# Performance work log

Hardware: AMD Instinct MI355X
Metric: run time of the kernel (lower is better)

Reference implementation:

```python
import jax, jax.numpy as jnp
import numpy as np

N_BITS = 8
QMAX = 2 ** (N_BITS - 1) - 1  # 127 for int8 symmetric


def fake_quant(x):
    """Per-token (last-dim) dynamic symmetric fake quantization (quant->dequant)."""
    scale = jnp.max(jnp.abs(x), axis=-1, keepdims=True) / QMAX
    scale = jnp.maximum(scale, 1e-8)
    q = jnp.clip(jnp.round(x / scale), -QMAX - 1, QMAX)
    return q * scale


def setup_inputs() -> dict:
    key = jax.random.key(0)
    k1, k2, k3, k4, k5 = jax.random.split(key, 5)
    B, T, D, H = 32, 1024, 1152, 4608
    x = jax.random.normal(k1, (B, T, D), dtype=jnp.float32)
    reorder_index = jnp.arange(D, dtype=jnp.int32)  # channel reorder permutation
    W1 = jax.random.normal(k2, (H, D), dtype=jnp.float32) * (1.0 / np.sqrt(D))
    b1 = jax.random.normal(k3, (H,), dtype=jnp.float32) * 0.02
    W2 = jax.random.normal(k4, (D, H), dtype=jnp.float32) * (1.0 / np.sqrt(H))
    b2 = jax.random.normal(k5, (D,), dtype=jnp.float32) * 0.02
    return {"x": x, "reorder_index": reorder_index, "W1": W1, "b1": b1, "W2": W2, "b2": b2}


def reference(x, reorder_index, W1, b1, W2, b2):
    # channel reorder (index_select on dim 2)
    x = jnp.take(x, reorder_index, axis=2)
    # input fake-quant
    x = fake_quant(x)
    # fc1 (torch Linear: x @ W.T + b)
    h = jnp.einsum("btd,hd->bth", x, W1) + b1
    # GELU activation (timm Mlp default); drop1/norm are Identity in eval
    h = jax.nn.gelu(h, approximate=False)
    # activation fake-quant
    h = fake_quant(h)
    # fc2
    out = jnp.einsum("bth,dh->btd", h, W2) + b2
    return out
```

## Files before the change

kernel.cpp:

```cpp
#include <hip/hip_runtime.h>
#include <cstdint>
#include <cstddef>


typedef __attribute__((ext_vector_type(8))) short short8;
typedef __attribute__((ext_vector_type(4))) float f32x4;

__device__ __forceinline__ float bf2f(unsigned short u) {
    return __uint_as_float(((unsigned)u) << 16);
}
__device__ __forceinline__ unsigned short f2bf(float f) {
    unsigned u = __float_as_uint(f);
    u += 0x7fff + ((u >> 16) & 1);
    return (unsigned short)(u >> 16);
}

__device__ __forceinline__ void gload_lds16(const void* gptr, void* ldsptr) {
    typedef __attribute__((address_space(1))) const unsigned int gu32;
    typedef __attribute__((address_space(3))) unsigned int lu32;
    __builtin_amdgcn_global_load_lds((gu32*)gptr, (lu32*)ldsptr, 16, 0, 0);
}

template <bool GELU>
__global__ __launch_bounds__(256) void gemm_bt(
    const unsigned short* __restrict__ A, const unsigned short* __restrict__ B,
    const float* __restrict__ bias, const float* __restrict__ rowScale,
    void* __restrict__ C, int M, int N, int K)
{
    __shared__ unsigned short lA[128 * 64];
    __shared__ unsigned short lB[128 * 64];

    const int tid  = threadIdx.x;
    const int lane = tid & 63;
    const int wave = tid >> 6;
    const int wm = wave >> 1;
    const int wn = wave & 1;
    const int bn = blockIdx.x;
    const int bm = blockIdx.y;

    const unsigned short* Ab = A + (size_t)bm * 128 * K;
    const unsigned short* Bb = B + (size_t)bn * 128 * K;

    f32x4 acc[4][4];
    const f32x4 zero = {0.f, 0.f, 0.f, 0.f};
#pragma unroll
    for (int i = 0; i < 4; ++i)
#pragma unroll
        for (int j = 0; j < 4; ++j) acc[i][j] = zero;

    const int q  = lane >> 4;
    const int lr = lane & 15;
    const int wbase = tid & 0xFFC0;

    const int nk = K >> 6;
    for (int kb = 0; kb < nk; ++kb) {
        const unsigned short* Ak = Ab + kb * 64;
        const unsigned short* Bk = Bb + kb * 64;
#pragma unroll
        for (int i = 0; i < 4; ++i) {
            int idx = i * 256 + tid;
            int r = idx >> 3, sc = idx & 7;
            int c = (sc ^ (r & 7)) << 3;
            gload_lds16(Ak + (size_t)r * K + c, &lA[(i * 256 + wbase) * 8]);
        }
#pragma unroll
        for (int i = 0; i < 4; ++i) {
            int idx = i * 256 + tid;
            int r = idx >> 3, sc = idx & 7;
            int c = (sc ^ (r & 7)) << 3;
            gload_lds16(Bk + (size_t)r * K + c, &lB[(i * 256 + wbase) * 8]);
        }
        __syncthreads();

#pragma unroll
        for (int ks = 0; ks < 2; ++ks) {
            short8 af[4], bfr[4];
            const int c8 = ks * 4 + q;
#pragma unroll
            for (int i = 0; i < 4; ++i) {
                int R = wm * 64 + i * 16 + lr;
                af[i] = *(const short8*)&lA[R * 64 + ((c8 ^ (R & 7)) << 3)];
            }
#pragma unroll
            for (int j = 0; j < 4; ++j) {
                int R = wn * 64 + j * 16 + lr;
                bfr[j] = *(const short8*)&lB[R * 64 + ((c8 ^ (R & 7)) << 3)];
            }
#pragma unroll
            for (int i = 0; i < 4; ++i)
#pragma unroll
                for (int j = 0; j < 4; ++j)
                    acc[i][j] = __builtin_amdgcn_mfma_f32_16x16x32_bf16(
                        af[i], bfr[j], acc[i][j], 0, 0, 0);
        }
        __syncthreads();
    }

#pragma unroll
    for (int i = 0; i < 4; ++i) {
#pragma unroll
        for (int r = 0; r < 4; ++r) {
            int m = bm * 128 + wm * 64 + i * 16 + q * 4 + r;
            float sc = rowScale[m];
#pragma unroll
            for (int j = 0; j < 4; ++j) {
                int n = bn * 128 + wn * 64 + j * 16 + lr;
                float v = acc[i][j][r] * sc + bias[n];
                size_t off = (size_t)m * N + n;
                if (GELU) {
                    v = 0.5f * v * (1.f + erff(v * 0.70710678118654752f));
                    ((unsigned short*)C)[off] = f2bf(v);
                } else {
                    ((float*)C)[off] = v;
                }
            }
        }
    }
}

__device__ __forceinline__ float waveMax(float m) {
#pragma unroll
    for (int off = 32; off; off >>= 1) m = fmaxf(m, __shfl_xor(m, off));
    return m;
}

__global__ __launch_bounds__(256) void quant_x_kernel(
    const float* __restrict__ x, const int* __restrict__ ridx,
    unsigned short* __restrict__ xq, float* __restrict__ sx, int D)
{
    __shared__ float buf[1152];
    __shared__ float wmax[4];
    const float* xr = x + (size_t)blockIdx.x * D;
    const int tid = threadIdx.x;
    float m = 0.f;
    for (int c = tid; c < D; c += 256) {
        float v = xr[ridx[c]];
        buf[c] = v;
        m = fmaxf(m, fabsf(v));
    }
    m = waveMax(m);
    if ((tid & 63) == 0) wmax[tid >> 6] = m;
    __syncthreads();
    m = fmaxf(fmaxf(wmax[0], wmax[1]), fmaxf(wmax[2], wmax[3]));
    float scale = fmaxf(m * (1.f / 127.f), 1e-8f);
    float inv = 1.f / scale;
    unsigned short* xo = xq + (size_t)blockIdx.x * D;
    for (int c = tid; c < D; c += 256) {
        float qv = fminf(fmaxf(rintf(buf[c] * inv), -128.f), 127.f);
        xo[c] = f2bf(qv);
    }
    if (tid == 0) sx[blockIdx.x] = scale;
}

__global__ __launch_bounds__(256) void quant_h_kernel(
    unsigned short* __restrict__ h, float* __restrict__ sh, int H)
{
    __shared__ float buf[4608];
    __shared__ float wmax[4];
    unsigned int* hr = (unsigned int*)(h + (size_t)blockIdx.x * H);
    const int tid = threadIdx.x;
    const int n2 = H >> 1;
    float m = 0.f;
    for (int c = tid; c < n2; c += 256) {
        unsigned int u = hr[c];
        float v0 = bf2f((unsigned short)(u & 0xffffu));
        float v1 = bf2f((unsigned short)(u >> 16));
        buf[2 * c] = v0; buf[2 * c + 1] = v1;
        m = fmaxf(m, fmaxf(fabsf(v0), fabsf(v1)));
    }
    m = waveMax(m);
    if ((tid & 63) == 0) wmax[tid >> 6] = m;
    __syncthreads();
    m = fmaxf(fmaxf(wmax[0], wmax[1]), fmaxf(wmax[2], wmax[3]));
    float scale = fmaxf(m * (1.f / 127.f), 1e-8f);
    float inv = 1.f / scale;
    for (int c = tid; c < n2; c += 256) {
        float q0 = fminf(fmaxf(rintf(buf[2 * c] * inv), -128.f), 127.f);
        float q1 = fminf(fmaxf(rintf(buf[2 * c + 1] * inv), -128.f), 127.f);
        hr[c] = (unsigned int)f2bf(q0) | ((unsigned int)f2bf(q1) << 16);
    }
    if (tid == 0) sh[blockIdx.x] = scale;
}

__global__ __launch_bounds__(256) void cvt_f32_bf16(
    const float* __restrict__ src, unsigned short* __restrict__ dst, long long n)
{
    long long i = ((long long)blockIdx.x * 256 + threadIdx.x) * 4;
    long long stride = (long long)gridDim.x * 1024;
    for (; i < n; i += stride) {
        float4 v = *(const float4*)(src + i);
        ushort4 o;
        o.x = f2bf(v.x); o.y = f2bf(v.y); o.z = f2bf(v.z); o.w = f2bf(v.w);
        *(ushort4*)(dst + i) = o;
    }
}

extern "C" void kernel_launch(void* const* d_in, const int* in_sizes, int n_in,
                              void* d_out, int out_size, void* d_ws, size_t ws_size,
                              hipStream_t stream)
{
    const float* x    = (const float*)d_in[0];
    const int*   ridx = (const int*)d_in[1];
    const float* W1   = (const float*)d_in[2];
    const float* b1   = (const float*)d_in[3];
    const float* W2   = (const float*)d_in[4];
    const float* b2   = (const float*)d_in[5];
    float* out = (float*)d_out;

    const long long D = in_sizes[1];
    const long long H = in_sizes[3];
    const long long M = (long long)in_sizes[0] / D;

    auto al = [](size_t v) { return (v + 255) & ~(size_t)255; };
    char* p = (char*)d_ws;
    unsigned short* w1b = (unsigned short*)p; p += al((size_t)(H * D * 2));
    unsigned short* w2b = (unsigned short*)p; p += al((size_t)(D * H * 2));
    size_t used = (size_t)(p - (char*)d_ws);

    size_t perTok = (size_t)(D + H) * 2 + 8;
    long long chunk = (long long)((ws_size - used - 4096) / perTok);
    chunk = (chunk / 128) * 128;
    if (chunk > M) chunk = M;
    if (chunk < 128) chunk = 128;

    unsigned short* xq   = (unsigned short*)p; p += al((size_t)chunk * D * 2);
    unsigned short* hbuf = (unsigned short*)p; p += al((size_t)chunk * H * 2);
    float* sx = (float*)p; p += al((size_t)chunk * 4);
    float* sh = (float*)p;

    cvt_f32_bf16<<<dim3((unsigned)((H * D) / 1024)), 256, 0, stream>>>(W1, w1b, H * D);
    cvt_f32_bf16<<<dim3((unsigned)((D * H) / 1024)), 256, 0, stream>>>(W2, w2b, D * H);

    for (long long r0 = 0; r0 < M; r0 += chunk) {
        long long mc = M - r0; if (mc > chunk) mc = chunk;
        quant_x_kernel<<<dim3((unsigned)mc), 256, 0, stream>>>(
            x + r0 * D, ridx, xq, sx, (int)D);
        gemm_bt<true><<<dim3((unsigned)(H / 128), (unsigned)(mc / 128)), 256, 0, stream>>>(
            xq, w1b, b1, sx, hbuf, (int)mc, (int)H, (int)D);
        quant_h_kernel<<<dim3((unsigned)mc), 256, 0, stream>>>(hbuf, sh, (int)H);
        gemm_bt<false><<<dim3((unsigned)(D / 128), (unsigned)(mc / 128)), 256, 0, stream>>>(
            hbuf, w2b, b2, sh, out + r0 * D, (int)mc, (int)D, (int)H);
    }
}
```

Before: 1.524 ms.

## Replace GEMM with 256-row, 8-wave, double-buffered pipelined kernel with XCD remap

The simple 128x128 single-buffered GEMM becomes an 8-wave kernel with 256-row tiles (256 or 128 columns). LDS is split into double-buffered half-K slabs, so global-to-LDS loads for later k-tiles are interleaved with MFMA phases using explicit waitcnt, barriers and setprio. A workgroup-index remap groups neighbouring tiles on the same XCD for L2 reuse, and chunk sizes round to 256 rows. This targets load latency and sync stalls and improves data reuse. The cost is high register pressure, hand-tuned vmcnt counts that must match the load schedule exactly, and the need for K to be a multiple of 128.

```diff
diff --git a/kernel.cpp b/kernel.cpp
--- a/kernel.cpp
+++ b/kernel.cpp
@@ -21,91 +21,146 @@
     __builtin_amdgcn_global_load_lds((gu32*)gptr, (lu32*)ldsptr, 16, 0, 0);
 }
 
-template <bool GELU>
-__global__ __launch_bounds__(256) void gemm_bt(
+template <int BN, bool GELU>
+__global__ __launch_bounds__(512, 2) void gemm8p(
     const unsigned short* __restrict__ A, const unsigned short* __restrict__ B,
     const float* __restrict__ bias, const float* __restrict__ rowScale,
     void* __restrict__ C, int M, int N, int K)
 {
-    __shared__ unsigned short lA[128 * 64];
-    __shared__ unsigned short lB[128 * 64];
+    constexpr int BM  = 256;
+    constexpr int NR  = BN / 64;
+    constexpr int WCN = BN / 4;
+    constexpr int LB  = (BN * 32 * 2) / (512 * 16);
+
+    __shared__ unsigned short lA[2][2][BM * 32];
+    __shared__ unsigned short lB[2][2][BN * 32];
 
     const int tid  = threadIdx.x;
     const int lane = tid & 63;
     const int wave = tid >> 6;
-    const int wm = wave >> 1;
-    const int wn = wave & 1;
-    const int bn = blockIdx.x;
-    const int bm = blockIdx.y;
-
-    const unsigned short* Ab = A + (size_t)bm * 128 * K;
-    const unsigned short* Bb = B + (size_t)bn * 128 * K;
-
-    f32x4 acc[4][4];
-    const f32x4 zero = {0.f, 0.f, 0.f, 0.f};
-#pragma unroll
-    for (int i = 0; i < 4; ++i)
-#pragma unroll
-        for (int j = 0; j < 4; ++j) acc[i][j] = zero;
+    const int wm = wave >> 2;
+    const int wn = wave & 3;
+    const int wbase = wave << 6;
+
+    const int nbn = N / BN;
+    {
+    }
+    const int nwg = (int)gridDim.x;
+    const int orig = (int)blockIdx.x;
+    const int qs = nwg >> 3, rs = nwg & 7;
+    const int xcd = orig & 7, loc = orig >> 3;
+    const int wg = (xcd < rs ? xcd * (qs + 1) : rs * (qs + 1) + (xcd - rs) * qs) + loc;
+    const int bn = wg % nbn;
+    const int bm = wg / nbn;
+
+    const unsigned short* Ab = A + (size_t)bm * BM * K;
+    const unsigned short* Bb = B + (size_t)bn * BN * K;
+
+    int srcA0, srcA1;
+    {
+        int idx = tid;       int r = idx >> 2, s = idx & 3;
+        srcA0 = r * K + ((s ^ ((r >> 1) & 3)) << 3);
+        idx = 512 + tid;     r = idx >> 2; s = idx & 3;
+        srcA1 = r * K + ((s ^ ((r >> 1) & 3)) << 3);
+    }
+
+    auto stageA = [&](unsigned short* slab, int t, int kh) {
+        const int ko = t * 64 + kh * 32;
+        gload_lds16(Ab + srcA0 + ko, &slab[wbase * 8]);
+        gload_lds16(Ab + srcA1 + ko, &slab[(512 + wbase) * 8]);
+    };
+    auto stageB = [&](unsigned short* slab, int t, int kh) {
+        const int ko = t * 64 + kh * 32;
+        gload_lds16(Bb + srcA0 + ko, &slab[wbase * 8]);
+        if (LB == 2) gload_lds16(Bb + srcA1 + ko, &slab[(512 + wbase) * 8]);
+    };
 
     const int q  = lane >> 4;
     const int lr = lane & 15;
-    const int wbase = tid & 0xFFC0;
-
-    const int nk = K >> 6;
-    for (int kb = 0; kb < nk; ++kb) {
-        const unsigned short* Ak = Ab + kb * 64;
-        const unsigned short* Bk = Bb + kb * 64;
-#pragma unroll
-        for (int i = 0; i < 4; ++i) {
-            int idx = i * 256 + tid;
-            int r = idx >> 3, sc = idx & 7;
-            int c = (sc ^ (r & 7)) << 3;
-            gload_lds16(Ak + (size_t)r * K + c, &lA[(i * 256 + wbase) * 8]);
-        }
-#pragma unroll
-        for (int i = 0; i < 4; ++i) {
-            int idx = i * 256 + tid;
-            int r = idx >> 3, sc = idx & 7;
-            int c = (sc ^ (r & 7)) << 3;
-            gload_lds16(Bk + (size_t)r * K + c, &lB[(i * 256 + wbase) * 8]);
-        }
-        __syncthreads();
-
-#pragma unroll
-        for (int ks = 0; ks < 2; ++ks) {
-            short8 af[4], bfr[4];
-            const int c8 = ks * 4 + q;
-#pragma unroll
-            for (int i = 0; i < 4; ++i) {
-                int R = wm * 64 + i * 16 + lr;
-                af[i] = *(const short8*)&lA[R * 64 + ((c8 ^ (R & 7)) << 3)];
-            }
-#pragma unroll
-            for (int j = 0; j < 4; ++j) {
-                int R = wn * 64 + j * 16 + lr;
-                bfr[j] = *(const short8*)&lB[R * 64 + ((c8 ^ (R & 7)) << 3)];
-            }
-#pragma unroll
-            for (int i = 0; i < 4; ++i)
-#pragma unroll
-                for (int j = 0; j < 4; ++j)
-                    acc[i][j] = __builtin_amdgcn_mfma_f32_16x16x32_bf16(
-                        af[i], bfr[j], acc[i][j], 0, 0, 0);
-        }
-        __syncthreads();
-    }
-
-#pragma unroll
-    for (int i = 0; i < 4; ++i) {
+    const int cidx = q ^ ((lr >> 1) & 3);
+    const int laneOff = lr * 32 + cidx * 8;
+
+    f32x4 acc[8][NR];
+#pragma unroll
+    for (int i = 0; i < 8; ++i)
+#pragma unroll
+        for (int j = 0; j < NR; ++j) acc[i][j] = (f32x4){0.f, 0.f, 0.f, 0.f};
+
+    short8 bfrag[NR];
+
+#define VM_WAIT()                                                            \
+    do { if (BN == 256) asm volatile("s_waitcnt vmcnt(6)" ::: "memory");     \
+         else           asm volatile("s_waitcnt vmcnt(4)" ::: "memory"); } while (0)
+
+#define PH(RD, RKH, MH, STG_A, SD, SKH, STGT, VM_END)                                  \
+    {                                                                                  \
+        short8 af[4];                                                                  \
+        if (MH == 0) {                                                                 \
+            _Pragma("unroll")                                                          \
+            for (int jj = 0; jj < NR; ++jj)                                            \
+                bfrag[jj] = *(const short8*)&lB[RD][RKH][(wn * WCN + jj * 16) * 32 + laneOff]; \
+        }                                                                              \
+        _Pragma("unroll")                                                              \
+        for (int ii = 0; ii < 4; ++ii)                                                 \
+            af[ii] = *(const short8*)&lA[RD][RKH][(wm * 128 + MH * 64 + ii * 16) * 32 + laneOff]; \
+        if (STG_A) stageA(&lA[SD][SKH][0], STGT, SKH);                                 \
+        else       stageB(&lB[SD][SKH][0], STGT, SKH);                                 \
+        asm volatile("" ::: "memory");                                                 \
+        __builtin_amdgcn_s_barrier();                                                  \
+        asm volatile("s_waitcnt lgkmcnt(0)" ::: "memory");                             \
+        __builtin_amdgcn_s_setprio(1);                                                 \
+        _Pragma("unroll")                                                              \
+        for (int ii = 0; ii < 4; ++ii)                                                 \
+            _Pragma("unroll")                                                          \
+            for (int jj = 0; jj < NR; ++jj)                                            \
+                acc[MH * 4 + ii][jj] = __builtin_amdgcn_mfma_f32_16x16x32_bf16(        \
+                    af[ii], bfrag[jj], acc[MH * 4 + ii][jj], 0, 0, 0);                 \
+        __builtin_amdgcn_s_setprio(0);                                                 \
+        if (VM_END) VM_WAIT();                                                         \
+        asm volatile("" ::: "memory");                                                 \
+        __builtin_amdgcn_s_barrier();                                                  \
+    }
+
+    const int nt = K >> 6;
+    const int nIter = nt >> 1;
+
+    stageB(&lB[0][0][0], 0, 0);
+    stageA(&lA[0][0][0], 0, 0);
+    stageB(&lB[0][1][0], 0, 1);
+    stageA(&lA[0][1][0], 0, 1);
+    stageB(&lB[1][0][0], 1, 0);
+    stageA(&lA[1][0][0], 1, 0);
+    stageB(&lB[1][1][0], 1, 1);
+    VM_WAIT();
+    asm volatile("" ::: "memory");
+    __builtin_amdgcn_s_barrier();
+
+    for (int it = 0; it < nIter; ++it) {
+        const int T  = it << 1;
+        const int t2 = (T + 2 < nt) ? T + 2 : nt - 1;
+        const int t3 = (T + 3 < nt) ? T + 3 : nt - 1;
+        PH(0, 0, 0, true , 1, 1, T + 1, false)
+        PH(0, 0, 1, false, 0, 0, t2,    false)
+        PH(0, 1, 0, true , 0, 0, t2,    false)
+        PH(0, 1, 1, false, 0, 1, t2,    true )
+        PH(1, 0, 0, true , 0, 1, t2,    false)
+        PH(1, 0, 1, false, 1, 0, t3,    false)
+        PH(1, 1, 0, true , 1, 0, t3,    false)
+        PH(1, 1, 1, false, 1, 1, t3,    true )
+    }
+#undef PH
+#undef VM_WAIT
+
+#pragma unroll
+    for (int mi = 0; mi < 8; ++mi) {
 #pragma unroll
         for (int r = 0; r < 4; ++r) {
-            int m = bm * 128 + wm * 64 + i * 16 + q * 4 + r;
+            int m = bm * BM + wm * 128 + mi * 16 + q * 4 + r;
             float sc = rowScale[m];
 #pragma unroll
-            for (int j = 0; j < 4; ++j) {
-                int n = bn * 128 + wn * 64 + j * 16 + lr;
-                float v = acc[i][j][r] * sc + bias[n];
+            for (int j = 0; j < NR; ++j) {
+                int n = bn * BN + wn * WCN + j * 16 + lr;
+                float v = acc[mi][j][r] * sc + bias[n];
                 size_t off = (size_t)m * N + n;
                 if (GELU) {
                     v = 0.5f * v * (1.f + erff(v * 0.70710678118654752f));
@@ -219,9 +274,9 @@
 
     size_t perTok = (size_t)(D + H) * 2 + 8;
     long long chunk = (long long)((ws_size - used - 4096) / perTok);
-    chunk = (chunk / 128) * 128;
+    chunk = (chunk / 256) * 256;
     if (chunk > M) chunk = M;
-    if (chunk < 128) chunk = 128;
+    if (chunk < 256) chunk = 256;
 
     unsigned short* xq   = (unsigned short*)p; p += al((size_t)chunk * D * 2);
     unsigned short* hbuf = (unsigned short*)p; p += al((size_t)chunk * H * 2);
@@ -235,10 +290,12 @@
         long long mc = M - r0; if (mc > chunk) mc = chunk;
         quant_x_kernel<<<dim3((unsigned)mc), 256, 0, stream>>>(
             x + r0 * D, ridx, xq, sx, (int)D);
-        gemm_bt<true><<<dim3((unsigned)(H / 128), (unsigned)(mc / 128)), 256, 0, stream>>>(
+        unsigned nwg1 = (unsigned)((H / 256) * (mc / 256));
+        gemm8p<256, true><<<dim3(nwg1), 512, 0, stream>>>(
             xq, w1b, b1, sx, hbuf, (int)mc, (int)H, (int)D);
         quant_h_kernel<<<dim3((unsigned)mc), 256, 0, stream>>>(hbuf, sh, (int)H);
-        gemm_bt<false><<<dim3((unsigned)(D / 128), (unsigned)(mc / 128)), 256, 0, stream>>>(
+        unsigned nwg2 = (unsigned)((D / 128) * (mc / 256));
+        gemm8p<128, false><<<dim3(nwg2), 512, 0, stream>>>(
             hbuf, w2b, b2, sh, out + r0 * D, (int)mc, (int)D, (int)H);
     }
 }
```

Result: no change. 1.503 ms (-1.4%).
